# Kernel optimization log

Measured on AMD Instinct MI355X. Metric: run time of the kernel, lower is better.

The kernel has to match this reference:

```python
import jax, jax.numpy as jnp
import numpy as np

T_FRAMES = 8
BN_EPS = 1e-3


def _depthwise_conv1d(x, w, b):
    # x: (M, C, T), w: (C, 1, 3) depthwise kernel, b: (C,)
    C = x.shape[1]
    y = jax.lax.conv_general_dilated(
        x, w, window_strides=(1,), padding=[(1, 1)],
        feature_group_count=C,
        dimension_numbers=("NCH", "OIH", "NCH"))
    return y + b[None, :, None]


def setup_inputs() -> dict:
    key = jax.random.key(0)
    ks = jax.random.split(key, 12)
    C, Cr = 64, 16  # dim, dim // TEA_ratio
    NT, H, W = 128, 56, 56
    inp = {
        "x": jax.random.normal(ks[0], (NT, C, H, W), dtype=jnp.float32),
        # depthwise temporal convs (Conv1d, groups=C, k=3)
        "shift_w": jax.random.normal(ks[1], (C, 1, 3), dtype=jnp.float32) * 0.3,
        "shift_b": jax.random.normal(ks[2], (C,), dtype=jnp.float32) * 0.1,
        "gate_w": jax.random.normal(ks[3], (C, 1, 3), dtype=jnp.float32) * 0.3,
        "gate_b": jax.random.normal(ks[4], (C,), dtype=jnp.float32) * 0.1,
        # BatchNorm1d (eval-mode running stats)
        "bn_gamma": jnp.ones((C,), dtype=jnp.float32),
        "bn_beta": jnp.zeros((C,), dtype=jnp.float32),
        "bn_mean": jax.random.normal(ks[5], (C,), dtype=jnp.float32) * 0.1,
        "bn_var": jax.random.uniform(ks[6], (C,), dtype=jnp.float32, minval=0.5, maxval=1.5),
        # TEA 1x1 convs stored as dense matrices
        "sq_w": jax.random.normal(ks[7], (Cr, C), dtype=jnp.float32) * 0.1,
        "sq_b": jax.random.normal(ks[8], (Cr,), dtype=jnp.float32) * 0.1,
        "ex_w": jax.random.normal(ks[9], (C, Cr), dtype=jnp.float32) * 0.1,
        "ex_b": jax.random.normal(ks[10], (C,), dtype=jnp.float32) * 0.1,
    }
    return inp


def reference(x, shift_w, shift_b, gate_w, gate_b,
              bn_gamma, bn_beta, bn_mean, bn_var,
              sq_w, sq_b, ex_w, ex_b):
    NT, C, H, W = x.shape
    T = T_FRAMES
    N = NT // T
    Cr = sq_w.shape[0]

    # ---- MotionExcitation ----
    # 1x1 squeeze conv: (NT, C, H, W) -> (NT, Cr, H, W)
    xs = jnp.einsum("nchw,kc->nkhw", x, sq_w) + sq_b[None, :, None, None]
    xr = xs.reshape(N, T, Cr, H, W)
    # diff = first frame - frames[:-1], zero-padded at the end (as in source)
    diff = xr[:, :1] - xr[:, :-1]                      # (N, T-1, Cr, H, W)
    diff = jnp.concatenate(
        [diff, jnp.zeros((N, 1, Cr, H, W), dtype=x.dtype)], axis=1)
    diff = diff.reshape(NT, Cr, H, W)
    gap = diff.mean(axis=(2, 3))                       # (NT, Cr)  global avg pool
    att = jax.nn.sigmoid(gap @ ex_w.T + ex_b)          # (NT, C)   expand + sigmoid
    S = x * att[:, :, None, None] + x                  # residual * att + residual

    # ---- Learnable temporal shift ----
    def to_ct(z):
        # (NT, C, H, W) -> (N, T, C, H, W) -> (N, H, W, C, T) -> (N*H*W, C, T)
        return z.reshape(N, T, C, H, W).transpose(0, 3, 4, 2, 1).reshape(-1, C, T)

    Sc = _depthwise_conv1d(to_ct(S), shift_w, shift_b)
    Gc = _depthwise_conv1d(to_ct(x), gate_w, gate_b)
    inv = bn_gamma * jax.lax.rsqrt(bn_var + BN_EPS)
    Gc = (Gc - bn_mean[None, :, None]) * inv[None, :, None] + bn_beta[None, :, None]
    out = Sc * jax.nn.sigmoid(Gc)                      # (N*H*W, C, T)

    out = out.reshape(N, H, W, C, T).transpose(0, 4, 3, 1, 2).reshape(NT, C, H, W)
    return out
```

## Files before the change

### kernel.cpp

```cpp
#include <hip/hip_runtime.h>
#include <math.h>

#define CDIM 64
#define CR 16
#define TFR 8
#define NBATCH 16
#define NTOT 128
#define HWPIX 3136
#define HW4 784

typedef float floatx4 __attribute__((ext_vector_type(4)));

__global__ __launch_bounds__(256) void spatial_mean_kernel(
    const float* __restrict__ x, float* __restrict__ xbar) {
  const int b = blockIdx.x;
  const float4* xp = reinterpret_cast<const float4*>(x + (size_t)b * HWPIX);
  float s = 0.f;
  for (int i = threadIdx.x; i < HW4; i += 256) {
    float4 v = xp[i];
    s += (v.x + v.y) + (v.z + v.w);
  }
  #pragma unroll
  for (int off = 32; off > 0; off >>= 1) s += __shfl_down(s, off, 64);
  __shared__ float wsum[4];
  const int lane = threadIdx.x & 63, wid = threadIdx.x >> 6;
  if (lane == 0) wsum[wid] = s;
  __syncthreads();
  if (threadIdx.x == 0) {
    float tot = (wsum[0] + wsum[1]) + (wsum[2] + wsum[3]);
    xbar[b] = tot * (1.0f / (float)HWPIX);
  }
}

__global__ __launch_bounds__(256) void fused_shift_kernel(
    const float* __restrict__ x,
    const float* __restrict__ xbar,
    const float* __restrict__ sq_w,
    const float* __restrict__ ex_w,
    const float* __restrict__ ex_b,
    const float* __restrict__ shift_w, const float* __restrict__ shift_b,
    const float* __restrict__ gate_w,  const float* __restrict__ gate_b,
    const float* __restrict__ bn_gamma, const float* __restrict__ bn_beta,
    const float* __restrict__ bn_mean,  const float* __restrict__ bn_var,
    float* __restrict__ out) {
  const int n = blockIdx.x >> 6;
  const int c = blockIdx.x & (CDIM - 1);
  const int tid = threadIdx.x;

  __shared__ float dsh[TFR][CDIM];
  __shared__ float gap[TFR][CR];
  __shared__ float attp1_sh[TFR];
  {
    const int base0 = (n * TFR) * CDIM;
    for (int i = tid; i < TFR * CDIM; i += 256) {
      const int t = i >> 6, cc = i & (CDIM - 1);
      dsh[t][cc] = (t == TFR - 1) ? 0.f : (xbar[base0 + cc] - xbar[base0 + t * CDIM + cc]);
    }
  }
  __syncthreads();
  if (tid < TFR * CR) {
    const int t = tid >> 4, k = tid & (CR - 1);
    float g = 0.f;
    #pragma unroll
    for (int cc = 0; cc < CDIM; ++cc) g += sq_w[k * CDIM + cc] * dsh[t][cc];
    gap[t][k] = g;
  }
  __syncthreads();
  if (tid < TFR) {
    float a = ex_b[c];
    #pragma unroll
    for (int k = 0; k < CR; ++k) a += ex_w[c * CR + k] * gap[tid][k];
    attp1_sh[tid] = 1.f + 1.f / (1.f + __expf(-a));
  }
  __syncthreads();

  const float sw0 = shift_w[c * 3 + 0], sw1 = shift_w[c * 3 + 1],
              sw2 = shift_w[c * 3 + 2], sb = shift_b[c];
  const float inv = bn_gamma[c] * rsqrtf(bn_var[c] + 1e-3f);
  const float g0 = gate_w[c * 3 + 0] * inv, g1 = gate_w[c * 3 + 1] * inv,
              g2 = gate_w[c * 3 + 2] * inv;
  const float gbias = (gate_b[c] - bn_mean[c]) * inv + bn_beta[c];

  float ap1[TFR];
  #pragma unroll
  for (int t = 0; t < TFR; ++t) ap1[t] = attp1_sh[t];

  const size_t base_nc = ((size_t)(n * TFR) * CDIM + c) * HWPIX;
  const size_t tstride = (size_t)CDIM * HWPIX;
  const float4 zero4 = make_float4(0.f, 0.f, 0.f, 0.f);

  for (int i = tid; i < HW4; i += 256) {
    const size_t off = base_nc + (size_t)i * 4;
    float4 xv[TFR], Sv[TFR];
    #pragma unroll
    for (int t = 0; t < TFR; ++t) {
      xv[t] = *reinterpret_cast<const float4*>(x + off + (size_t)t * tstride);
      Sv[t].x = xv[t].x * ap1[t];
      Sv[t].y = xv[t].y * ap1[t];
      Sv[t].z = xv[t].z * ap1[t];
      Sv[t].w = xv[t].w * ap1[t];
    }
    #pragma unroll
    for (int t = 0; t < TFR; ++t) {
      const float4 Sm = (t > 0) ? Sv[t - 1] : zero4;
      const float4 Sp = (t < TFR - 1) ? Sv[t + 1] : zero4;
      const float4 xm = (t > 0) ? xv[t - 1] : zero4;
      const float4 xp = (t < TFR - 1) ? xv[t + 1] : zero4;
      floatx4 o;
      {
        const float sc = sb + sw0 * Sm.x + sw1 * Sv[t].x + sw2 * Sp.x;
        const float gc = gbias + g0 * xm.x + g1 * xv[t].x + g2 * xp.x;
        o.x = sc * (1.f / (1.f + __expf(-gc)));
      }
      {
        const float sc = sb + sw0 * Sm.y + sw1 * Sv[t].y + sw2 * Sp.y;
        const float gc = gbias + g0 * xm.y + g1 * xv[t].y + g2 * xp.y;
        o.y = sc * (1.f / (1.f + __expf(-gc)));
      }
      {
        const float sc = sb + sw0 * Sm.z + sw1 * Sv[t].z + sw2 * Sp.z;
        const float gc = gbias + g0 * xm.z + g1 * xv[t].z + g2 * xp.z;
        o.z = sc * (1.f / (1.f + __expf(-gc)));
      }
      {
        const float sc = sb + sw0 * Sm.w + sw1 * Sv[t].w + sw2 * Sp.w;
        const float gc = gbias + g0 * xm.w + g1 * xv[t].w + g2 * xp.w;
        o.w = sc * (1.f / (1.f + __expf(-gc)));
      }
      __builtin_nontemporal_store(
          o, reinterpret_cast<floatx4*>(out + off + (size_t)t * tstride));
    }
  }
}

extern "C" void kernel_launch(void* const* d_in, const int* in_sizes, int n_in,
                              void* d_out, int out_size, void* d_ws, size_t ws_size,
                              hipStream_t stream) {
  const float* x        = (const float*)d_in[0];
  const float* shift_w  = (const float*)d_in[1];
  const float* shift_b  = (const float*)d_in[2];
  const float* gate_w   = (const float*)d_in[3];
  const float* gate_b   = (const float*)d_in[4];
  const float* bn_gamma = (const float*)d_in[5];
  const float* bn_beta  = (const float*)d_in[6];
  const float* bn_mean  = (const float*)d_in[7];
  const float* bn_var   = (const float*)d_in[8];
  const float* sq_w     = (const float*)d_in[9];
  const float* ex_w     = (const float*)d_in[11];
  const float* ex_b     = (const float*)d_in[12];
  float* out = (float*)d_out;

  float* xbar = (float*)d_ws;

  spatial_mean_kernel<<<NTOT * CDIM, 256, 0, stream>>>(x, xbar);
  fused_shift_kernel<<<NBATCH * CDIM, 256, 0, stream>>>(
      x, xbar, sq_w, ex_w, ex_b, shift_w, shift_b, gate_w, gate_b,
      bn_gamma, bn_beta, bn_mean, bn_var, out);
}
```

Before: 58.25 us.

## Precompute fused excite-squeeze matrix, prefetch next tile, drop nontemporal stores

An extra block in the mean kernel precomputes M = ex_w·sq_w. The shift kernel can then compute each attention logit directly as a dot product of a row of M with the mean differences, which removes two shared-memory stages and three block barriers. The main loop now software-pipelines the x loads, issuing the loads for the next 256-pixel chunk before computing the current one. The output writes also change from nontemporal stores to ordinary stores. The aim is to hide load latency and shorten the per-block prologue, at the cost of more registers (16 float4 buffers) and a redundant per-thread 64-element dot product for every timestep.

```diff
diff --git a/kernel.cpp b/kernel.cpp
--- a/kernel.cpp
+++ b/kernel.cpp
@@ -9,11 +9,23 @@
 #define HWPIX 3136
 #define HW4 784
 
-typedef float floatx4 __attribute__((ext_vector_type(4)));
-
-__global__ __launch_bounds__(256) void spatial_mean_kernel(
-    const float* __restrict__ x, float* __restrict__ xbar) {
+__global__ __launch_bounds__(256) void mean_and_M_kernel(
+    const float* __restrict__ x,
+    const float* __restrict__ sq_w,
+    const float* __restrict__ ex_w,
+    float* __restrict__ xbar,
+    float* __restrict__ M) {
   const int b = blockIdx.x;
+  if (b == NTOT * CDIM) {
+    for (int e = threadIdx.x; e < CDIM * CDIM; e += 256) {
+      const int c = e >> 6, cc = e & (CDIM - 1);
+      float m = 0.f;
+      #pragma unroll
+      for (int k = 0; k < CR; ++k) m += ex_w[c * CR + k] * sq_w[k * CDIM + cc];
+      M[e] = m;
+    }
+    return;
+  }
   const float4* xp = reinterpret_cast<const float4*>(x + (size_t)b * HWPIX);
   float s = 0.f;
   for (int i = threadIdx.x; i < HW4; i += 256) {
@@ -35,8 +47,7 @@
 __global__ __launch_bounds__(256) void fused_shift_kernel(
     const float* __restrict__ x,
     const float* __restrict__ xbar,
-    const float* __restrict__ sq_w,
-    const float* __restrict__ ex_w,
+    const float* __restrict__ M,
     const float* __restrict__ ex_b,
     const float* __restrict__ shift_w, const float* __restrict__ shift_b,
     const float* __restrict__ gate_w,  const float* __restrict__ gate_b,
@@ -47,32 +58,33 @@
   const int c = blockIdx.x & (CDIM - 1);
   const int tid = threadIdx.x;
 
-  __shared__ float dsh[TFR][CDIM];
-  __shared__ float gap[TFR][CR];
-  __shared__ float attp1_sh[TFR];
+  const size_t base_nc = ((size_t)(n * TFR) * CDIM + c) * HWPIX;
+  const size_t tstride = (size_t)CDIM * HWPIX;
+
+  int i = tid;
+  float4 cur[TFR];
+  #pragma unroll
+  for (int t = 0; t < TFR; ++t)
+    cur[t] = *reinterpret_cast<const float4*>(x + base_nc + (size_t)i * 4 +
+                                              (size_t)t * tstride);
+
+  const float a07 = ex_b[c];
+  float ap1[TFR];
   {
-    const int base0 = (n * TFR) * CDIM;
-    for (int i = tid; i < TFR * CDIM; i += 256) {
-      const int t = i >> 6, cc = i & (CDIM - 1);
-      dsh[t][cc] = (t == TFR - 1) ? 0.f : (xbar[base0 + cc] - xbar[base0 + t * CDIM + cc]);
+    const float* Mr = M + c * CDIM;
+    const float* xb0 = xbar + (n * TFR) * CDIM;
+    float a[TFR];
+    a[0] = a07; a[TFR - 1] = a07;
+    #pragma unroll
+    for (int t = 1; t < TFR - 1; ++t) {
+      float s = a07;
+      const float* xbt = xb0 + t * CDIM;
+      for (int cc = 0; cc < CDIM; ++cc) s += Mr[cc] * (xb0[cc] - xbt[cc]);
+      a[t] = s;
     }
+    #pragma unroll
+    for (int t = 0; t < TFR; ++t) ap1[t] = 1.f + 1.f / (1.f + __expf(-a[t]));
   }
-  __syncthreads();
-  if (tid < TFR * CR) {
-    const int t = tid >> 4, k = tid & (CR - 1);
-    float g = 0.f;
-    #pragma unroll
-    for (int cc = 0; cc < CDIM; ++cc) g += sq_w[k * CDIM + cc] * dsh[t][cc];
-    gap[t][k] = g;
-  }
-  __syncthreads();
-  if (tid < TFR) {
-    float a = ex_b[c];
-    #pragma unroll
-    for (int k = 0; k < CR; ++k) a += ex_w[c * CR + k] * gap[tid][k];
-    attp1_sh[tid] = 1.f + 1.f / (1.f + __expf(-a));
-  }
-  __syncthreads();
 
   const float sw0 = shift_w[c * 3 + 0], sw1 = shift_w[c * 3 + 1],
               sw2 = shift_w[c * 3 + 2], sb = shift_b[c];
@@ -81,55 +93,62 @@
               g2 = gate_w[c * 3 + 2] * inv;
   const float gbias = (gate_b[c] - bn_mean[c]) * inv + bn_beta[c];
 
-  float ap1[TFR];
-  #pragma unroll
-  for (int t = 0; t < TFR; ++t) ap1[t] = attp1_sh[t];
-
-  const size_t base_nc = ((size_t)(n * TFR) * CDIM + c) * HWPIX;
-  const size_t tstride = (size_t)CDIM * HWPIX;
   const float4 zero4 = make_float4(0.f, 0.f, 0.f, 0.f);
 
-  for (int i = tid; i < HW4; i += 256) {
-    const size_t off = base_nc + (size_t)i * 4;
-    float4 xv[TFR], Sv[TFR];
+  while (true) {
+    const int nx = i + 256;
+    const bool has_next = (nx < HW4);
+    float4 nxt[TFR];
+    if (has_next) {
+      #pragma unroll
+      for (int t = 0; t < TFR; ++t)
+        nxt[t] = *reinterpret_cast<const float4*>(x + base_nc + (size_t)nx * 4 +
+                                                  (size_t)t * tstride);
+    }
+
+    float4 Sv[TFR];
     #pragma unroll
     for (int t = 0; t < TFR; ++t) {
-      xv[t] = *reinterpret_cast<const float4*>(x + off + (size_t)t * tstride);
-      Sv[t].x = xv[t].x * ap1[t];
-      Sv[t].y = xv[t].y * ap1[t];
-      Sv[t].z = xv[t].z * ap1[t];
-      Sv[t].w = xv[t].w * ap1[t];
+      Sv[t].x = cur[t].x * ap1[t];
+      Sv[t].y = cur[t].y * ap1[t];
+      Sv[t].z = cur[t].z * ap1[t];
+      Sv[t].w = cur[t].w * ap1[t];
     }
+    const size_t off = base_nc + (size_t)i * 4;
     #pragma unroll
     for (int t = 0; t < TFR; ++t) {
       const float4 Sm = (t > 0) ? Sv[t - 1] : zero4;
       const float4 Sp = (t < TFR - 1) ? Sv[t + 1] : zero4;
-      const float4 xm = (t > 0) ? xv[t - 1] : zero4;
-      const float4 xp = (t < TFR - 1) ? xv[t + 1] : zero4;
-      floatx4 o;
+      const float4 xm = (t > 0) ? cur[t - 1] : zero4;
+      const float4 xp = (t < TFR - 1) ? cur[t + 1] : zero4;
+      float4 o;
       {
         const float sc = sb + sw0 * Sm.x + sw1 * Sv[t].x + sw2 * Sp.x;
-        const float gc = gbias + g0 * xm.x + g1 * xv[t].x + g2 * xp.x;
+        const float gc = gbias + g0 * xm.x + g1 * cur[t].x + g2 * xp.x;
         o.x = sc * (1.f / (1.f + __expf(-gc)));
       }
       {
         const float sc = sb + sw0 * Sm.y + sw1 * Sv[t].y + sw2 * Sp.y;
-        const float gc = gbias + g0 * xm.y + g1 * xv[t].y + g2 * xp.y;
+        const float gc = gbias + g0 * xm.y + g1 * cur[t].y + g2 * xp.y;
         o.y = sc * (1.f / (1.f + __expf(-gc)));
       }
       {
         const float sc = sb + sw0 * Sm.z + sw1 * Sv[t].z + sw2 * Sp.z;
-        const float gc = gbias + g0 * xm.z + g1 * xv[t].z + g2 * xp.z;
+        const float gc = gbias + g0 * xm.z + g1 * cur[t].z + g2 * xp.z;
         o.z = sc * (1.f / (1.f + __expf(-gc)));
       }
       {
         const float sc = sb + sw0 * Sm.w + sw1 * Sv[t].w + sw2 * Sp.w;
-        const float gc = gbias + g0 * xm.w + g1 * xv[t].w + g2 * xp.w;
+        const float gc = gbias + g0 * xm.w + g1 * cur[t].w + g2 * xp.w;
         o.w = sc * (1.f / (1.f + __expf(-gc)));
       }
-      __builtin_nontemporal_store(
-          o, reinterpret_cast<floatx4*>(out + off + (size_t)t * tstride));
+      *reinterpret_cast<float4*>(out + off + (size_t)t * tstride) = o;
     }
+
+    if (!has_next) break;
+    i = nx;
+    #pragma unroll
+    for (int t = 0; t < TFR; ++t) cur[t] = nxt[t];
   }
 }
 
@@ -151,9 +170,10 @@
   float* out = (float*)d_out;
 
   float* xbar = (float*)d_ws;
+  float* M    = (float*)d_ws + NTOT * CDIM;
 
-  spatial_mean_kernel<<<NTOT * CDIM, 256, 0, stream>>>(x, xbar);
+  mean_and_M_kernel<<<NTOT * CDIM + 1, 256, 0, stream>>>(x, sq_w, ex_w, xbar, M);
   fused_shift_kernel<<<NBATCH * CDIM, 256, 0, stream>>>(
-      x, xbar, sq_w, ex_w, ex_b, shift_w, shift_b, gate_w, gate_b,
+      x, xbar, M, ex_b, shift_w, shift_b, gate_w, gate_b,
       bn_gamma, bn_beta, bn_mean, bn_var, out);
 }
```

After: 70.21 us. 20.5% more time.
